# Kernel optimization log

Measured on AMD Instinct MI355X. Metric: run time of the kernel, lower is better.

## Reference

```python
import jax, jax.numpy as jnp
import numpy as np

N_NODES = 50000
N_EDGES = 1600000
CHANNELS = 128
EXPANSION = 50
CUTOFF = 5.0
LOG2 = 0.6931471805599453


def shifted_softplus(x):
    return jax.nn.softplus(x) - LOG2


def gaussian_smearing(r, cutoff=CUTOFF, n=EXPANSION):
    # centers evenly spaced in [0, cutoff]; width set by spacing
    centers = jnp.linspace(0.0, cutoff, n, dtype=r.dtype)
    delta = centers[1] - centers[0]
    coef = 1.0 / (2.0 * delta * delta)
    d = r[:, None] - centers[None, :]          # [E, n]
    return jnp.exp(-coef * d * d)


def setup_inputs() -> dict:
    key = jax.random.key(0)
    ks = jax.random.split(key, 12)
    C, F = CHANNELS, EXPANSION

    def lin(k, fan_in, shape):
        bound = 1.0 / np.sqrt(fan_in)
        return jax.random.uniform(k, shape, jnp.float32, -bound, bound)

    return {
        "features": jax.random.normal(ks[0], (N_NODES, C), jnp.float32),
        "edge_distances": jax.random.uniform(ks[1], (N_EDGES,), jnp.float32) * CUTOFF,
        "W_lin": lin(ks[2], C, (C, C)),
        "Wf1": lin(ks[3], F, (F, C)), "bf1": lin(ks[4], F, (C,)),
        "Wf2": lin(ks[5], C, (C, C)), "bf2": lin(ks[6], C, (C,)),
        "Wm1": lin(ks[7], C, (C, C)), "bm1": lin(ks[8], C, (C,)),
        "Wm2": lin(ks[9], C, (C, C)), "bm2": lin(ks[10], C, (C,)),
        "senders": jax.random.randint(ks[11], (N_EDGES,), 0, N_NODES, jnp.int32),
        "receivers": jax.random.randint(jax.random.fold_in(key, 99), (N_EDGES,), 0, N_NODES, jnp.int32),
    }


def reference(features, edge_distances, W_lin, Wf1, bf1, Wf2, bf2,
              Wm1, bm1, Wm2, bm2, senders, receivers):
    # 1. linear transform of node features (no bias)
    h = features @ W_lin.T                                   # [N, C]
    # 2. learnable radial filter F(r_ij): Gaussian basis -> MLP
    basis = gaussian_smearing(edge_distances)                # [E, F]
    ef = shifted_softplus(basis @ Wf1 + bf1) @ Wf2 + bf2     # [E, C]
    # 3. gather neighbour features, elementwise multiply, scatter-sum
    messages = h[senders] * ef                               # [E, C]
    agg = jax.ops.segment_sum(messages, receivers, num_segments=N_NODES)  # [N, C]
    # 4. output MLP
    return shifted_softplus(agg @ Wm1 + bm1) @ Wm2 + bm2
```

## Files before the change

kernel.cpp:

```cpp
#include <hip/hip_runtime.h>
#include <hip/hip_bf16.h>
#include <math.h>

#define N_NODES 50000
#define N_EDGES 1600000
#define CH 128
#define NF 50
#define NR 8192
#define NB 1563
#define BUCKET_NODES 32
#define CAP 1280
#define PASSA_CHUNK 2048
#define NBLK_SCAT 782
#define NBLK_TB   128
#define NBLK_DH   782

constexpr float DELTA  = 5.0f / 49.0f;
constexpr float COEF   = 1.0f / (2.0f * DELTA * DELTA);
constexpr float LOG2_  = 0.6931471805599453f;
constexpr float RSCALE = (float)(NR - 1) / 5.0f;

typedef short  bf16x8 __attribute__((ext_vector_type(8)));
typedef float  f32x4  __attribute__((ext_vector_type(4)));
typedef unsigned short ushort_t;
typedef unsigned long long u64;

__device__ __forceinline__ float ssp(float x) {
    return fmaxf(x, 0.0f) + __logf(1.0f + __expf(-fabsf(x))) - LOG2_;
}
__device__ __forceinline__ ushort_t f2bf(float x) {
    __hip_bfloat16 b = __float2bfloat16(x);
    return *reinterpret_cast<ushort_t*>(&b);
}
__device__ __forceinline__ float bf2f(ushort_t u) {
    return __uint_as_float(((unsigned)u) << 16);
}
__device__ __forceinline__ float4 f4zero() { return make_float4(0.f, 0.f, 0.f, 0.f); }

__global__ __launch_bounds__(256) void k1_prep(const float* __restrict__ Wlin,
                                               const float* __restrict__ Wm1,
                                               const float* __restrict__ Wm2,
                                               const float* __restrict__ Wf1,
                                               const float* __restrict__ Wf2,
                                               ushort_t* __restrict__ wlhi,
                                               ushort_t* __restrict__ wllo,
                                               ushort_t* __restrict__ wm1hi,
                                               ushort_t* __restrict__ wm1lo,
                                               ushort_t* __restrict__ wm2hi,
                                               ushort_t* __restrict__ wm2lo,
                                               ushort_t* __restrict__ wf1t,
                                               ushort_t* __restrict__ wf2hi,
                                               ushort_t* __restrict__ wf2lo,
                                               int* __restrict__ bcnt) {
    const int tid = threadIdx.x;
    if (blockIdx.x == 64) {
        for (int i = tid; i < NB; i += 256) bcnt[i] = 0;
        return;
    }
    int idx = blockIdx.x * 256 + tid;
    int n = idx >> 7, k = idx & 127;
    {   float w = Wlin[(size_t)n * CH + k];
        ushort_t hi = f2bf(w); wlhi[n * CH + k] = hi; wllo[n * CH + k] = f2bf(w - bf2f(hi)); }
    {   float w = Wm1[(size_t)k * CH + n];
        ushort_t hi = f2bf(w); wm1hi[n * CH + k] = hi; wm1lo[n * CH + k] = f2bf(w - bf2f(hi)); }
    {   float w = Wm2[(size_t)k * CH + n];
        ushort_t hi = f2bf(w); wm2hi[n * CH + k] = hi; wm2lo[n * CH + k] = f2bf(w - bf2f(hi)); }
    if (k < 64) wf1t[n * 64 + k] = (k < NF) ? f2bf(Wf1[k * CH + n]) : (ushort_t)0;
    {   float w = Wf2[(size_t)k * CH + n];
        ushort_t hi = f2bf(w); wf2hi[n * CH + k] = hi; wf2lo[n * CH + k] = f2bf(w - bf2f(hi)); }
}

__device__ void scatter_body(char* smem, int blk,
                             const int* __restrict__ recv,
                             const int* __restrict__ send,
                             const float* __restrict__ dist,
                             int* __restrict__ bcnt,
                             u64* __restrict__ brec) {
    int* bcur   = (int*)smem;
    int* bbaseL = bcur + NB;
    const int tid = threadIdx.x;
    for (int i = tid; i < NB; i += 256) bcur[i] = 0;
    __syncthreads();
    const int e0 = blk * PASSA_CHUNK;
    const bool full = (e0 + PASSA_CHUNK <= N_EDGES);
    int r8[8];
    if (full) {
#pragma unroll
        for (int i = 0; i < 8; i++) r8[i] = recv[e0 + tid + i * 256];
#pragma unroll
        for (int i = 0; i < 8; i++) atomicAdd(&bcur[r8[i] / BUCKET_NODES], 1);
    } else {
#pragma unroll
        for (int i = 0; i < 8; i++) {
            int e = e0 + tid + i * 256;
            r8[i] = (e < N_EDGES) ? recv[e] : -1;
            if (r8[i] >= 0) atomicAdd(&bcur[r8[i] / BUCKET_NODES], 1);
        }
    }
    __syncthreads();
    for (int i = tid; i < NB; i += 256) {
        int c = bcur[i];
        bbaseL[i] = c ? atomicAdd(&bcnt[i], c) : 0;
        bcur[i] = 0;
    }
    __syncthreads();
    if (full) {
        int s8[8]; float d8[8];
#pragma unroll
        for (int i = 0; i < 8; i++) {
            int e = e0 + tid + i * 256;
            s8[i] = send[e];
            d8[i] = dist[e];
        }
#pragma unroll
        for (int i = 0; i < 8; i++) {
            int b = r8[i] / BUCKET_NODES;
            int rank = bbaseL[b] + atomicAdd(&bcur[b], 1);
            if (rank < CAP) {
                int ti = __float2int_rn(fminf(d8[i] * RSCALE, (float)(NR - 1)));
                u64 rec = (u64)(unsigned)(s8[i] | (r8[i] << 16)) | ((u64)ti << 32);
                brec[(size_t)b * CAP + rank] = rec;
            }
        }
    } else {
#pragma unroll
        for (int i = 0; i < 8; i++) {
            int e = e0 + tid + i * 256;
            if (e < N_EDGES) {
                int r = r8[i];
                int b = r / BUCKET_NODES;
                int rank = bbaseL[b] + atomicAdd(&bcur[b], 1);
                if (rank < CAP) {
                    int ti = __float2int_rn(fminf(dist[e] * RSCALE, (float)(NR - 1)));
                    u64 rec = (u64)(unsigned)(send[e] | (r << 16)) | ((u64)ti << 32);
                    brec[(size_t)b * CAP + rank] = rec;
                }
            }
        }
    }
}

__device__ void table_body(char* smem, int blk,
                           const float* __restrict__ bf1,
                           const float* __restrict__ bf2,
                           const ushort_t* __restrict__ wf1t,
                           const ushort_t* __restrict__ wf2hi,
                           const ushort_t* __restrict__ wf2lo,
                           ushort_t* __restrict__ tabn) {
    ushort_t (*basis)[72] = (ushort_t (*)[72])smem;
    ushort_t (*t1s)[136]  = (ushort_t (*)[136])(smem + 64 * 72 * 2);
    const int tid = threadIdx.x;
    const int g0  = blk * 64;

    for (int i = tid; i < 64 * 64; i += 256) {
        int e = i >> 6, k = i & 63;
        float val = 0.f;
        if (k < NF) {
            float r = (float)(g0 + e) * (5.0f / (float)(NR - 1));
            float d = r - (float)k * DELTA;
            val = __expf(-COEF * d * d);
        }
        basis[e][k] = f2bf(val);
    }
    __syncthreads();

    const int lane = tid & 63;
    const int wv   = tid >> 6;
    const int row  = lane & 15;
    const int quad = lane >> 4;
    const int c0   = (2 * wv) * 16 + row;
    const int c1   = c0 + 16;

    f32x4 acc[2][4];
#pragma unroll
    for (int j = 0; j < 2; j++)
#pragma unroll
        for (int rt = 0; rt < 4; rt++) acc[j][rt] = (f32x4){0.f, 0.f, 0.f, 0.f};

#pragma unroll
    for (int kb = 0; kb < 64; kb += 32) {
        bf16x8 B0 = *(const bf16x8*)&wf1t[c0 * 64 + kb + quad * 8];
        bf16x8 B1 = *(const bf16x8*)&wf1t[c1 * 64 + kb + quad * 8];
#pragma unroll
        for (int rt = 0; rt < 4; rt++) {
            bf16x8 A = *(const bf16x8*)&basis[rt * 16 + row][kb + quad * 8];
            acc[0][rt] = __builtin_amdgcn_mfma_f32_16x16x32_bf16(A, B0, acc[0][rt], 0, 0, 0);
            acc[1][rt] = __builtin_amdgcn_mfma_f32_16x16x32_bf16(A, B1, acc[1][rt], 0, 0, 0);
        }
    }
    {
        float b1v[2] = { bf1[c0], bf1[c1] };
#pragma unroll
        for (int j = 0; j < 2; j++) {
            int c = j ? c1 : c0;
#pragma unroll
            for (int rt = 0; rt < 4; rt++)
#pragma unroll
                for (int rg = 0; rg < 4; rg++) {
                    int e = rt * 16 + quad * 4 + rg;
                    t1s[e][c] = f2bf(ssp(acc[j][rt][rg] + b1v[j]));
                }
        }
    }
    __syncthreads();

#pragma unroll
    for (int j = 0; j < 2; j++)
#pragma unroll
        for (int rt = 0; rt < 4; rt++) acc[j][rt] = (f32x4){0.f, 0.f, 0.f, 0.f};

#pragma unroll
    for (int kb = 0; kb < 128; kb += 32) {
        bf16x8 B0h = *(const bf16x8*)&wf2hi[c0 * CH + kb + quad * 8];
        bf16x8 B0l = *(const bf16x8*)&wf2lo[c0 * CH + kb + quad * 8];
        bf16x8 B1h = *(const bf16x8*)&wf2hi[c1 * CH + kb + quad * 8];
        bf16x8 B1l = *(const bf16x8*)&wf2lo[c1 * CH + kb + quad * 8];
#pragma unroll
        for (int rt = 0; rt < 4; rt++) {
            bf16x8 A = *(const bf16x8*)&t1s[rt * 16 + row][kb + quad * 8];
            acc[0][rt] = __builtin_amdgcn_mfma_f32_16x16x32_bf16(A, B0l, acc[0][rt], 0, 0, 0);
            acc[0][rt] = __builtin_amdgcn_mfma_f32_16x16x32_bf16(A, B0h, acc[0][rt], 0, 0, 0);
            acc[1][rt] = __builtin_amdgcn_mfma_f32_16x16x32_bf16(A, B1l, acc[1][rt], 0, 0, 0);
            acc[1][rt] = __builtin_amdgcn_mfma_f32_16x16x32_bf16(A, B1h, acc[1][rt], 0, 0, 0);
        }
    }
    {
        float b2v[2] = { bf2[c0], bf2[c1] };
#pragma unroll
        for (int j = 0; j < 2; j++) {
            int c = j ? c1 : c0;
#pragma unroll
            for (int rt = 0; rt < 4; rt++)
#pragma unroll
                for (int rg = 0; rg < 4; rg++) {
                    int g = g0 + rt * 16 + quad * 4 + rg;
                    tabn[(size_t)g * CH + c] = f2bf(acc[j][rt][rg] + b2v[j]);
                }
        }
    }
}

__device__ void dense_h_body(char* smem, int blk,
                             const float* __restrict__ X,
                             const ushort_t* __restrict__ Bhi,
                             const ushort_t* __restrict__ Blo,
                             ushort_t* __restrict__ Y) {
    ushort_t (*xs)[136] = (ushort_t (*)[136])smem;
    const int tid  = threadIdx.x;
    const int row0 = blk * 64;

#pragma unroll
    for (int i = 0; i < 8; i++) {
        int idx = tid + i * 256;
        int r   = idx >> 5;
        int c4  = (idx & 31) * 4;
        float4 v = (row0 + r < N_NODES) ? *(const float4*)&X[(size_t)(row0 + r) * CH + c4]
                                        : f4zero();
        ushort4 s;
        s.x = f2bf(v.x); s.y = f2bf(v.y); s.z = f2bf(v.z); s.w = f2bf(v.w);
        *(ushort4*)&xs[r][c4] = s;
    }
    __syncthreads();

    const int lane = tid & 63;
    const int wv   = tid >> 6;
    const int row  = lane & 15;
    const int quad = lane >> 4;
    const int c0   = (2 * wv) * 16 + row;
    const int c1   = c0 + 16;

    f32x4 acc[2][4];
#pragma unroll
    for (int j = 0; j < 2; j++)
#pragma unroll
        for (int rt = 0; rt < 4; rt++) acc[j][rt] = (f32x4){0.f, 0.f, 0.f, 0.f};

#pragma unroll
    for (int kb = 0; kb < 128; kb += 32) {
        bf16x8 B0h = *(const bf16x8*)&Bhi[(size_t)c0 * CH + kb + quad * 8];
        bf16x8 B0l = *(const bf16x8*)&Blo[(size_t)c0 * CH + kb + quad * 8];
        bf16x8 B1h = *(const bf16x8*)&Bhi[(size_t)c1 * CH + kb + quad * 8];
        bf16x8 B1l = *(const bf16x8*)&Blo[(size_t)c1 * CH + kb + quad * 8];
#pragma unroll
        for (int rt = 0; rt < 4; rt++) {
            bf16x8 A = *(const bf16x8*)&xs[rt * 16 + row][kb + quad * 8];
            acc[0][rt] = __builtin_amdgcn_mfma_f32_16x16x32_bf16(A, B0l, acc[0][rt], 0, 0, 0);
            acc[0][rt] = __builtin_amdgcn_mfma_f32_16x16x32_bf16(A, B0h, acc[0][rt], 0, 0, 0);
            acc[1][rt] = __builtin_amdgcn_mfma_f32_16x16x32_bf16(A, B1l, acc[1][rt], 0, 0, 0);
            acc[1][rt] = __builtin_amdgcn_mfma_f32_16x16x32_bf16(A, B1h, acc[1][rt], 0, 0, 0);
        }
    }

#pragma unroll
    for (int j = 0; j < 2; j++) {
        int c = j ? c1 : c0;
#pragma unroll
        for (int rt = 0; rt < 4; rt++)
#pragma unroll
            for (int rg = 0; rg < 4; rg++) {
                int r = row0 + rt * 16 + quad * 4 + rg;
                if (r < N_NODES) Y[(size_t)r * CH + c] = f2bf(acc[j][rt][rg]);
            }
    }
}

__global__ __launch_bounds__(256) void k2_mega(const int* __restrict__ recv,
                                               const int* __restrict__ send,
                                               const float* __restrict__ dist,
                                               int* __restrict__ bcnt,
                                               u64* __restrict__ brec,
                                               const float* __restrict__ bf1,
                                               const float* __restrict__ bf2,
                                               const ushort_t* __restrict__ wf1t,
                                               const ushort_t* __restrict__ wf2hi,
                                               const ushort_t* __restrict__ wf2lo,
                                               ushort_t* __restrict__ tabn,
                                               const float* __restrict__ X,
                                               const ushort_t* __restrict__ wlhi,
                                               const ushort_t* __restrict__ wllo,
                                               ushort_t* __restrict__ h) {
    __shared__ __align__(16) char smem[64 * 72 * 2 + 64 * 136 * 2];
    const int blk = blockIdx.x;
    if (blk < NBLK_SCAT) {
        scatter_body(smem, blk, recv, send, dist, bcnt, brec);
    } else if (blk < NBLK_SCAT + NBLK_TB) {
        table_body(smem, blk - NBLK_SCAT, bf1, bf2, wf1t, wf2hi, wf2lo, tabn);
    } else {
        dense_h_body(smem, blk - NBLK_SCAT - NBLK_TB, X, wlhi, wllo, h);
    }
}

__global__ __launch_bounds__(256) void sort_gather_mlp(const int* __restrict__ bcnt,
                                                       const u64* __restrict__ brec,
                                                       const ushort_t* __restrict__ h,
                                                       const ushort_t* __restrict__ tabn,
                                                       const ushort_t* __restrict__ B1hi,
                                                       const ushort_t* __restrict__ B1lo,
                                                       const float* __restrict__ bm1,
                                                       const ushort_t* __restrict__ B2hi,
                                                       const ushort_t* __restrict__ B2lo,
                                                       const float* __restrict__ bm2,
                                                       float* __restrict__ OUT) {
    __shared__ int shist[BUCKET_NODES];
    __shared__ int sbeg[BUCKET_NODES];
    __shared__ int sexc[BUCKET_NODES];
    __shared__ unsigned sout[CAP];
    __shared__ __align__(16) ushort_t at[32][136];
    const int b = blockIdx.x, tid = threadIdx.x;
    const int nbase = b * BUCKET_NODES;
    const int nn = min(BUCKET_NODES, N_NODES - nbase);
    if (nn <= 0) return;
    const int m = min(bcnt[b], CAP);
    const u64* my = brec + (size_t)b * CAP;

    if (tid < BUCKET_NODES) shist[tid] = 0;
    for (int i = tid; i < 32 * 17; i += 256) {
        bf16x8 z = (bf16x8){0, 0, 0, 0, 0, 0, 0, 0};
        *(bf16x8*)&at[i / 17][(i % 17) * 8] = z;
    }
    __syncthreads();
    for (int i = tid; i < m; i += 256) {
        u64 rec = my[i];
        int l = (int)((rec >> 16) & 0xFFFF) - nbase;
        atomicAdd(&shist[l], 1);
    }
    __syncthreads();
    if (tid == 0) {
        int acc = 0;
#pragma unroll
        for (int l = 0; l < BUCKET_NODES; l++) {
            if (l < nn) { sexc[l] = acc; sbeg[l] = acc; acc += shist[l]; }
        }
    }
    __syncthreads();
    for (int i = tid; i < m; i += 256) {
        u64 rec = my[i];
        int l = (int)((rec >> 16) & 0xFFFF) - nbase;
        int rank = atomicAdd(&sexc[l], 1);
        sout[rank] = (unsigned)(rec & 0xFFFF) | ((unsigned)((rec >> 32) & 0x3FFF) << 16);
    }
    __syncthreads();

    {
        const int g  = tid >> 4;
        const int c8 = (tid & 15) * 8;
        for (int l = g; l < nn; l += 16) {
            const int beg = sbeg[l], end = sbeg[l] + shist[l];
            float acc[8];
#pragma unroll
            for (int j = 0; j < 8; j++) acc[j] = 0.f;

            int e = beg;
            for (; e + 8 <= end; e += 8) {
                unsigned v[8];
#pragma unroll
                for (int u = 0; u < 8; u++) v[u] = sout[e + u];
                bf16x8 hu[8], tn[8];
#pragma unroll
                for (int u = 0; u < 8; u++) {
                    int s  = (int)(v[u] & 0xFFFF);
                    int ti = (int)(v[u] >> 16);
                    hu[u] = *(const bf16x8*)&h[(size_t)s * CH + c8];
                    tn[u] = *(const bf16x8*)&tabn[(size_t)ti * CH + c8];
                }
#pragma unroll
                for (int u = 0; u < 8; u++)
#pragma unroll
                    for (int j = 0; j < 8; j++)
                        acc[j] = fmaf(bf2f((ushort_t)hu[u][j]), bf2f((ushort_t)tn[u][j]), acc[j]);
            }
            for (; e + 4 <= end; e += 4) {
                unsigned v[4];
#pragma unroll
                for (int u = 0; u < 4; u++) v[u] = sout[e + u];
                bf16x8 hu[4], tn[4];
#pragma unroll
                for (int u = 0; u < 4; u++) {
                    int s  = (int)(v[u] & 0xFFFF);
                    int ti = (int)(v[u] >> 16);
                    hu[u] = *(const bf16x8*)&h[(size_t)s * CH + c8];
                    tn[u] = *(const bf16x8*)&tabn[(size_t)ti * CH + c8];
                }
#pragma unroll
                for (int u = 0; u < 4; u++)
#pragma unroll
                    for (int j = 0; j < 8; j++)
                        acc[j] = fmaf(bf2f((ushort_t)hu[u][j]), bf2f((ushort_t)tn[u][j]), acc[j]);
            }
            for (; e < end; e++) {
                unsigned v = sout[e];
                int s  = (int)(v & 0xFFFF);
                int ti = (int)(v >> 16);
                bf16x8 hu = *(const bf16x8*)&h[(size_t)s * CH + c8];
                bf16x8 tn = *(const bf16x8*)&tabn[(size_t)ti * CH + c8];
#pragma unroll
                for (int j = 0; j < 8; j++)
                    acc[j] = fmaf(bf2f((ushort_t)hu[j]), bf2f((ushort_t)tn[j]), acc[j]);
            }

            bf16x8 o;
#pragma unroll
            for (int j = 0; j < 8; j++) o[j] = (short)f2bf(acc[j]);
            *(bf16x8*)&at[l][c8] = o;
        }
    }
    __syncthreads();

    const int lane = tid & 63;
    const int wv   = tid >> 6;
    const int row  = lane & 15;
    const int quad = lane >> 4;
    const int c0   = (2 * wv) * 16 + row;
    const int c1   = c0 + 16;

    f32x4 acc[2][2];
#pragma unroll
    for (int j = 0; j < 2; j++)
#pragma unroll
        for (int rt = 0; rt < 2; rt++) acc[j][rt] = (f32x4){0.f, 0.f, 0.f, 0.f};

#pragma unroll
    for (int kb = 0; kb < 128; kb += 32) {
        bf16x8 B0h = *(const bf16x8*)&B1hi[(size_t)c0 * CH + kb + quad * 8];
        bf16x8 B0l = *(const bf16x8*)&B1lo[(size_t)c0 * CH + kb + quad * 8];
        bf16x8 B1h_ = *(const bf16x8*)&B1hi[(size_t)c1 * CH + kb + quad * 8];
        bf16x8 B1l_ = *(const bf16x8*)&B1lo[(size_t)c1 * CH + kb + quad * 8];
#pragma unroll
        for (int rt = 0; rt < 2; rt++) {
            bf16x8 A = *(const bf16x8*)&at[rt * 16 + row][kb + quad * 8];
            acc[0][rt] = __builtin_amdgcn_mfma_f32_16x16x32_bf16(A, B0l, acc[0][rt], 0, 0, 0);
            acc[0][rt] = __builtin_amdgcn_mfma_f32_16x16x32_bf16(A, B0h, acc[0][rt], 0, 0, 0);
            acc[1][rt] = __builtin_amdgcn_mfma_f32_16x16x32_bf16(A, B1l_, acc[1][rt], 0, 0, 0);
            acc[1][rt] = __builtin_amdgcn_mfma_f32_16x16x32_bf16(A, B1h_, acc[1][rt], 0, 0, 0);
        }
    }
    __syncthreads();
    {
        float bv[2] = { bm1[c0], bm1[c1] };
#pragma unroll
        for (int j = 0; j < 2; j++) {
            int c = j ? c1 : c0;
#pragma unroll
            for (int rt = 0; rt < 2; rt++)
#pragma unroll
                for (int rg = 0; rg < 4; rg++)
                    at[rt * 16 + quad * 4 + rg][c] = f2bf(ssp(acc[j][rt][rg] + bv[j]));
        }
    }
    __syncthreads();

#pragma unroll
    for (int j = 0; j < 2; j++)
#pragma unroll
        for (int rt = 0; rt < 2; rt++) acc[j][rt] = (f32x4){0.f, 0.f, 0.f, 0.f};

#pragma unroll
    for (int kb = 0; kb < 128; kb += 32) {
        bf16x8 B0h = *(const bf16x8*)&B2hi[(size_t)c0 * CH + kb + quad * 8];
        bf16x8 B0l = *(const bf16x8*)&B2lo[(size_t)c0 * CH + kb + quad * 8];
        bf16x8 B1h_ = *(const bf16x8*)&B2hi[(size_t)c1 * CH + kb + quad * 8];
        bf16x8 B1l_ = *(const bf16x8*)&B2lo[(size_t)c1 * CH + kb + quad * 8];
#pragma unroll
        for (int rt = 0; rt < 2; rt++) {
            bf16x8 A = *(const bf16x8*)&at[rt * 16 + row][kb + quad * 8];
            acc[0][rt] = __builtin_amdgcn_mfma_f32_16x16x32_bf16(A, B0l, acc[0][rt], 0, 0, 0);
            acc[0][rt] = __builtin_amdgcn_mfma_f32_16x16x32_bf16(A, B0h, acc[0][rt], 0, 0, 0);
            acc[1][rt] = __builtin_amdgcn_mfma_f32_16x16x32_bf16(A, B1l_, acc[1][rt], 0, 0, 0);
            acc[1][rt] = __builtin_amdgcn_mfma_f32_16x16x32_bf16(A, B1h_, acc[1][rt], 0, 0, 0);
        }
    }
    {
        float bv[2] = { bm2[c0], bm2[c1] };
#pragma unroll
        for (int j = 0; j < 2; j++) {
            int c = j ? c1 : c0;
#pragma unroll
            for (int rt = 0; rt < 2; rt++)
#pragma unroll
                for (int rg = 0; rg < 4; rg++) {
                    int r = rt * 16 + quad * 4 + rg;
                    if (r < nn) OUT[(size_t)(nbase + r) * CH + c] = acc[j][rt][rg] + bv[j];
                }
        }
    }
}

extern "C" void kernel_launch(void* const* d_in, const int* in_sizes, int n_in,
                              void* d_out, int out_size, void* d_ws, size_t ws_size,
                              hipStream_t stream) {
    const float* features = (const float*)d_in[0];
    const float* dist     = (const float*)d_in[1];
    const float* W_lin    = (const float*)d_in[2];
    const float* Wf1      = (const float*)d_in[3];
    const float* bf1      = (const float*)d_in[4];
    const float* Wf2      = (const float*)d_in[5];
    const float* bf2      = (const float*)d_in[6];
    const float* Wm1      = (const float*)d_in[7];
    const float* bm1      = (const float*)d_in[8];
    const float* Wm2      = (const float*)d_in[9];
    const float* bm2      = (const float*)d_in[10];
    const int* senders    = (const int*)d_in[11];
    const int* receivers  = (const int*)d_in[12];
    float* out = (float*)d_out;

    u64* brec       = (u64*)d_ws;
    ushort_t* h     = (ushort_t*)(brec + (size_t)NB * CAP);
    ushort_t* tabn  = h + (size_t)N_NODES * CH;
    int* bcnt       = (int*)(tabn + (size_t)NR * CH);
    ushort_t* wlhi  = (ushort_t*)(bcnt + NB);
    ushort_t* wllo  = wlhi  + CH * CH;
    ushort_t* wm1hi = wllo  + CH * CH;
    ushort_t* wm1lo = wm1hi + CH * CH;
    ushort_t* wm2hi = wm1lo + CH * CH;
    ushort_t* wm2lo = wm2hi + CH * CH;
    ushort_t* wf1t  = wm2lo + CH * CH;
    ushort_t* wf2hi = wf1t  + CH * 64;
    ushort_t* wf2lo = wf2hi + CH * CH;

    k1_prep<<<65, 256, 0, stream>>>(W_lin, Wm1, Wm2, Wf1, Wf2,
                                    wlhi, wllo, wm1hi, wm1lo, wm2hi, wm2lo,
                                    wf1t, wf2hi, wf2lo, bcnt);

    k2_mega<<<NBLK_SCAT + NBLK_TB + NBLK_DH, 256, 0, stream>>>(
        receivers, senders, dist, bcnt, brec,
        bf1, bf2, wf1t, wf2hi, wf2lo, tabn,
        features, wlhi, wllo, h);

    sort_gather_mlp<<<NB, 256, 0, stream>>>(bcnt, brec, h, tabn,
                                            wm1hi, wm1lo, bm1,
                                            wm2hi, wm2lo, bm2, out);
}
```

Baseline: 258.8 us.

## Halve bucket size to 16 nodes per block, one node per thread group

Shrinks each receiver bucket from 32 to 16 nodes, doubling the block count and cutting bucket capacity. Each group of 16 threads now handles exactly one node, so the strided node loop, the shared tile zeroing and the second MFMA row tile go away. The aim is more blocks in flight, less per-block shared memory and better latency hiding for the gather phase. The smaller CAP raises the chance that a bucket overflows and edges are silently dropped. Upstream bucketing kernels must also agree with the new NB and CAP.

```diff
diff --git a/kernel.cpp b/kernel.cpp
--- a/kernel.cpp
+++ b/kernel.cpp
@@ -7,9 +7,9 @@
 #define CH 128
 #define NF 50
 #define NR 8192
-#define NB 1563
-#define BUCKET_NODES 32
-#define CAP 1280
+#define NB 3125
+#define BUCKET_NODES 16
+#define CAP 704
 #define PASSA_CHUNK 2048
 #define NBLK_SCAT 782
 #define NBLK_TB   128
@@ -345,7 +345,7 @@
     __shared__ int sbeg[BUCKET_NODES];
     __shared__ int sexc[BUCKET_NODES];
     __shared__ unsigned sout[CAP];
-    __shared__ __align__(16) ushort_t at[32][136];
+    __shared__ __align__(16) ushort_t at[16][136];
     const int b = blockIdx.x, tid = threadIdx.x;
     const int nbase = b * BUCKET_NODES;
     const int nn = min(BUCKET_NODES, N_NODES - nbase);
@@ -354,10 +354,6 @@
     const u64* my = brec + (size_t)b * CAP;
 
     if (tid < BUCKET_NODES) shist[tid] = 0;
-    for (int i = tid; i < 32 * 17; i += 256) {
-        bf16x8 z = (bf16x8){0, 0, 0, 0, 0, 0, 0, 0};
-        *(bf16x8*)&at[i / 17][(i % 17) * 8] = z;
-    }
     __syncthreads();
     for (int i = tid; i < m; i += 256) {
         u64 rec = my[i];
@@ -369,7 +365,7 @@
         int acc = 0;
 #pragma unroll
         for (int l = 0; l < BUCKET_NODES; l++) {
-            if (l < nn) { sexc[l] = acc; sbeg[l] = acc; acc += shist[l]; }
+            sexc[l] = acc; sbeg[l] = acc; acc += shist[l];
         }
     }
     __syncthreads();
@@ -382,67 +378,65 @@
     __syncthreads();
 
     {
-        const int g  = tid >> 4;
+        const int l  = tid >> 4;
         const int c8 = (tid & 15) * 8;
-        for (int l = g; l < nn; l += 16) {
-            const int beg = sbeg[l], end = sbeg[l] + shist[l];
-            float acc[8];
-#pragma unroll
-            for (int j = 0; j < 8; j++) acc[j] = 0.f;
-
-            int e = beg;
-            for (; e + 8 <= end; e += 8) {
-                unsigned v[8];
-#pragma unroll
-                for (int u = 0; u < 8; u++) v[u] = sout[e + u];
-                bf16x8 hu[8], tn[8];
-#pragma unroll
-                for (int u = 0; u < 8; u++) {
-                    int s  = (int)(v[u] & 0xFFFF);
-                    int ti = (int)(v[u] >> 16);
-                    hu[u] = *(const bf16x8*)&h[(size_t)s * CH + c8];
-                    tn[u] = *(const bf16x8*)&tabn[(size_t)ti * CH + c8];
-                }
-#pragma unroll
-                for (int u = 0; u < 8; u++)
-#pragma unroll
-                    for (int j = 0; j < 8; j++)
-                        acc[j] = fmaf(bf2f((ushort_t)hu[u][j]), bf2f((ushort_t)tn[u][j]), acc[j]);
+        const int beg = sbeg[l], end = sbeg[l] + shist[l];
+        float acc[8];
+#pragma unroll
+        for (int j = 0; j < 8; j++) acc[j] = 0.f;
+
+        int e = beg;
+        for (; e + 8 <= end; e += 8) {
+            unsigned v[8];
+#pragma unroll
+            for (int u = 0; u < 8; u++) v[u] = sout[e + u];
+            bf16x8 hu[8], tn[8];
+#pragma unroll
+            for (int u = 0; u < 8; u++) {
+                int s  = (int)(v[u] & 0xFFFF);
+                int ti = (int)(v[u] >> 16);
+                hu[u] = *(const bf16x8*)&h[(size_t)s * CH + c8];
+                tn[u] = *(const bf16x8*)&tabn[(size_t)ti * CH + c8];
             }
-            for (; e + 4 <= end; e += 4) {
-                unsigned v[4];
-#pragma unroll
-                for (int u = 0; u < 4; u++) v[u] = sout[e + u];
-                bf16x8 hu[4], tn[4];
-#pragma unroll
-                for (int u = 0; u < 4; u++) {
-                    int s  = (int)(v[u] & 0xFFFF);
-                    int ti = (int)(v[u] >> 16);
-                    hu[u] = *(const bf16x8*)&h[(size_t)s * CH + c8];
-                    tn[u] = *(const bf16x8*)&tabn[(size_t)ti * CH + c8];
-                }
-#pragma unroll
-                for (int u = 0; u < 4; u++)
-#pragma unroll
-                    for (int j = 0; j < 8; j++)
-                        acc[j] = fmaf(bf2f((ushort_t)hu[u][j]), bf2f((ushort_t)tn[u][j]), acc[j]);
+#pragma unroll
+            for (int u = 0; u < 8; u++)
+#pragma unroll
+                for (int j = 0; j < 8; j++)
+                    acc[j] = fmaf(bf2f((ushort_t)hu[u][j]), bf2f((ushort_t)tn[u][j]), acc[j]);
+        }
+        for (; e + 4 <= end; e += 4) {
+            unsigned v[4];
+#pragma unroll
+            for (int u = 0; u < 4; u++) v[u] = sout[e + u];
+            bf16x8 hu[4], tn[4];
+#pragma unroll
+            for (int u = 0; u < 4; u++) {
+                int s  = (int)(v[u] & 0xFFFF);
+                int ti = (int)(v[u] >> 16);
+                hu[u] = *(const bf16x8*)&h[(size_t)s * CH + c8];
+                tn[u] = *(const bf16x8*)&tabn[(size_t)ti * CH + c8];
             }
-            for (; e < end; e++) {
-                unsigned v = sout[e];
-                int s  = (int)(v & 0xFFFF);
-                int ti = (int)(v >> 16);
-                bf16x8 hu = *(const bf16x8*)&h[(size_t)s * CH + c8];
-                bf16x8 tn = *(const bf16x8*)&tabn[(size_t)ti * CH + c8];
+#pragma unroll
+            for (int u = 0; u < 4; u++)
 #pragma unroll
                 for (int j = 0; j < 8; j++)
-                    acc[j] = fmaf(bf2f((ushort_t)hu[j]), bf2f((ushort_t)tn[j]), acc[j]);
-            }
-
-            bf16x8 o;
-#pragma unroll
-            for (int j = 0; j < 8; j++) o[j] = (short)f2bf(acc[j]);
-            *(bf16x8*)&at[l][c8] = o;
-        }
+                    acc[j] = fmaf(bf2f((ushort_t)hu[u][j]), bf2f((ushort_t)tn[u][j]), acc[j]);
+        }
+        for (; e < end; e++) {
+            unsigned v = sout[e];
+            int s  = (int)(v & 0xFFFF);
+            int ti = (int)(v >> 16);
+            bf16x8 hu = *(const bf16x8*)&h[(size_t)s * CH + c8];
+            bf16x8 tn = *(const bf16x8*)&tabn[(size_t)ti * CH + c8];
+#pragma unroll
+            for (int j = 0; j < 8; j++)
+                acc[j] = fmaf(bf2f((ushort_t)hu[j]), bf2f((ushort_t)tn[j]), acc[j]);
+        }
+
+        bf16x8 o;
+#pragma unroll
+        for (int j = 0; j < 8; j++) o[j] = (short)f2bf(acc[j]);
+        *(bf16x8*)&at[l][c8] = o;
     }
     __syncthreads();
 
@@ -453,11 +447,9 @@
     const int c0   = (2 * wv) * 16 + row;
     const int c1   = c0 + 16;
 
-    f32x4 acc[2][2];
-#pragma unroll
-    for (int j = 0; j < 2; j++)
-#pragma unroll
-        for (int rt = 0; rt < 2; rt++) acc[j][rt] = (f32x4){0.f, 0.f, 0.f, 0.f};
+    f32x4 acc0, acc1;
+    acc0 = (f32x4){0.f, 0.f, 0.f, 0.f};
+    acc1 = (f32x4){0.f, 0.f, 0.f, 0.f};
 
 #pragma unroll
     for (int kb = 0; kb < 128; kb += 32) {
@@ -465,34 +457,25 @@
         bf16x8 B0l = *(const bf16x8*)&B1lo[(size_t)c0 * CH + kb + quad * 8];
         bf16x8 B1h_ = *(const bf16x8*)&B1hi[(size_t)c1 * CH + kb + quad * 8];
         bf16x8 B1l_ = *(const bf16x8*)&B1lo[(size_t)c1 * CH + kb + quad * 8];
-#pragma unroll
-        for (int rt = 0; rt < 2; rt++) {
-            bf16x8 A = *(const bf16x8*)&at[rt * 16 + row][kb + quad * 8];
-            acc[0][rt] = __builtin_amdgcn_mfma_f32_16x16x32_bf16(A, B0l, acc[0][rt], 0, 0, 0);
-            acc[0][rt] = __builtin_amdgcn_mfma_f32_16x16x32_bf16(A, B0h, acc[0][rt], 0, 0, 0);
-            acc[1][rt] = __builtin_amdgcn_mfma_f32_16x16x32_bf16(A, B1l_, acc[1][rt], 0, 0, 0);
-            acc[1][rt] = __builtin_amdgcn_mfma_f32_16x16x32_bf16(A, B1h_, acc[1][rt], 0, 0, 0);
-        }
+        bf16x8 A = *(const bf16x8*)&at[row][kb + quad * 8];
+        acc0 = __builtin_amdgcn_mfma_f32_16x16x32_bf16(A, B0l, acc0, 0, 0, 0);
+        acc0 = __builtin_amdgcn_mfma_f32_16x16x32_bf16(A, B0h, acc0, 0, 0, 0);
+        acc1 = __builtin_amdgcn_mfma_f32_16x16x32_bf16(A, B1l_, acc1, 0, 0, 0);
+        acc1 = __builtin_amdgcn_mfma_f32_16x16x32_bf16(A, B1h_, acc1, 0, 0, 0);
     }
     __syncthreads();
     {
-        float bv[2] = { bm1[c0], bm1[c1] };
-#pragma unroll
-        for (int j = 0; j < 2; j++) {
-            int c = j ? c1 : c0;
-#pragma unroll
-            for (int rt = 0; rt < 2; rt++)
-#pragma unroll
-                for (int rg = 0; rg < 4; rg++)
-                    at[rt * 16 + quad * 4 + rg][c] = f2bf(ssp(acc[j][rt][rg] + bv[j]));
-        }
-    }
-    __syncthreads();
-
-#pragma unroll
-    for (int j = 0; j < 2; j++)
-#pragma unroll
-        for (int rt = 0; rt < 2; rt++) acc[j][rt] = (f32x4){0.f, 0.f, 0.f, 0.f};
+        float bv0 = bm1[c0], bv1 = bm1[c1];
+#pragma unroll
+        for (int rg = 0; rg < 4; rg++) {
+            at[quad * 4 + rg][c0] = f2bf(ssp(acc0[rg] + bv0));
+            at[quad * 4 + rg][c1] = f2bf(ssp(acc1[rg] + bv1));
+        }
+    }
+    __syncthreads();
+
+    acc0 = (f32x4){0.f, 0.f, 0.f, 0.f};
+    acc1 = (f32x4){0.f, 0.f, 0.f, 0.f};
 
 #pragma unroll
     for (int kb = 0; kb < 128; kb += 32) {
@@ -500,27 +483,21 @@
         bf16x8 B0l = *(const bf16x8*)&B2lo[(size_t)c0 * CH + kb + quad * 8];
         bf16x8 B1h_ = *(const bf16x8*)&B2hi[(size_t)c1 * CH + kb + quad * 8];
         bf16x8 B1l_ = *(const bf16x8*)&B2lo[(size_t)c1 * CH + kb + quad * 8];
-#pragma unroll
-        for (int rt = 0; rt < 2; rt++) {
-            bf16x8 A = *(const bf16x8*)&at[rt * 16 + row][kb + quad * 8];
-            acc[0][rt] = __builtin_amdgcn_mfma_f32_16x16x32_bf16(A, B0l, acc[0][rt], 0, 0, 0);
-            acc[0][rt] = __builtin_amdgcn_mfma_f32_16x16x32_bf16(A, B0h, acc[0][rt], 0, 0, 0);
-            acc[1][rt] = __builtin_amdgcn_mfma_f32_16x16x32_bf16(A, B1l_, acc[1][rt], 0, 0, 0);
-            acc[1][rt] = __builtin_amdgcn_mfma_f32_16x16x32_bf16(A, B1h_, acc[1][rt], 0, 0, 0);
-        }
+        bf16x8 A = *(const bf16x8*)&at[row][kb + quad * 8];
+        acc0 = __builtin_amdgcn_mfma_f32_16x16x32_bf16(A, B0l, acc0, 0, 0, 0);
+        acc0 = __builtin_amdgcn_mfma_f32_16x16x32_bf16(A, B0h, acc0, 0, 0, 0);
+        acc1 = __builtin_amdgcn_mfma_f32_16x16x32_bf16(A, B1l_, acc1, 0, 0, 0);
+        acc1 = __builtin_amdgcn_mfma_f32_16x16x32_bf16(A, B1h_, acc1, 0, 0, 0);
     }
     {
-        float bv[2] = { bm2[c0], bm2[c1] };
-#pragma unroll
-        for (int j = 0; j < 2; j++) {
-            int c = j ? c1 : c0;
-#pragma unroll
-            for (int rt = 0; rt < 2; rt++)
-#pragma unroll
-                for (int rg = 0; rg < 4; rg++) {
-                    int r = rt * 16 + quad * 4 + rg;
-                    if (r < nn) OUT[(size_t)(nbase + r) * CH + c] = acc[j][rt][rg] + bv[j];
-                }
+        float bv0 = bm2[c0], bv1 = bm2[c1];
+#pragma unroll
+        for (int rg = 0; rg < 4; rg++) {
+            int r = quad * 4 + rg;
+            if (r < nn) {
+                OUT[(size_t)(nbase + r) * CH + c0] = acc0[rg] + bv0;
+                OUT[(size_t)(nbase + r) * CH + c1] = acc1[rg] + bv1;
+            }
         }
     }
 }
```

New measurement: 285.3 us. 10.2% more time.
